# Optimization experiments

Hardware: AMD Instinct MI355X
Metric: run time of the kernel (lower is better)

The kernel has to match this reference:

```python
import jax, jax.numpy as jnp
import numpy as np

E, N, H, D = 800000, 50000, 4, 32
ATT_NORM = 4.0
EPS = 1e-12


def setup_inputs() -> dict:
    key = jax.random.key(0)
    k1, k2, k3, k4, k5 = jax.random.split(key, 5)
    x = jax.random.normal(k1, (E, H, D), dtype=jnp.float32)
    att_l = jax.random.normal(k2, (1, H, D), dtype=jnp.float32)
    att_r = jax.random.normal(k3, (1, H, D), dtype=jnp.float32)
    alpha = jax.random.normal(k4, (E, H), dtype=jnp.float32)
    index = jax.random.randint(k5, (E,), 0, N, dtype=jnp.int64)
    return {"x": x, "att_l": att_l, "att_r": att_r, "alpha": alpha,
            "index": index, "num_nodes": N}


def reference(x, att_l, att_r, alpha, index, num_nodes):
    # recenter=False -> no mean subtraction
    # ||x||^2 along feature dim: [E, H]
    norm_x = jnp.sum(x * x, axis=-1)
    # scatter-max over target nodes: [N, H]; empty segments -> 0 (torch zero-init)
    max_norm = jax.ops.segment_max(norm_x, index, num_segments=num_nodes)
    max_norm = jnp.where(jnp.isfinite(max_norm), max_norm, jnp.zeros_like(max_norm))
    # faithful to torch .view(-1, 1) then [index]: flatten [N,H] -> [N*H,1], gather rows
    max_norm_flat = max_norm.reshape(-1, 1)          # [N*H, 1]
    gathered = max_norm_flat[index]                  # [E, 1]
    max_norm_e = jnp.sqrt(gathered + norm_x)         # [E, H]
    # scale_individually=True: per-head norm of concatenated attention vectors
    att_cat = jnp.concatenate((att_l, att_r), axis=-1)        # [1, H, 2D]
    norm_att = ATT_NORM * jnp.linalg.norm(att_cat, axis=-1)   # [1, H]
    return alpha / (norm_att * max_norm_e + EPS)
```

## Files before the change

kernel.cpp:

```cpp
#include <hip/hip_runtime.h>
#include <math.h>


static constexpr int   H_        = 4;
static constexpr int   D_        = 32;
static constexpr int   N_NODES   = 50000;
static constexpr int   N_LIVE    = N_NODES / H_;
static constexpr float ATT_NORM_ = 4.0f;
static constexpr float EPS_      = 1e-12f;

__global__ void __launch_bounds__(256)
k_norm_scatter(const float* __restrict__ x,
               const int* __restrict__ index,
               const float* __restrict__ att_l,
               const float* __restrict__ att_r,
               float* __restrict__ max_norm,
               float* __restrict__ norm_x,
               float* __restrict__ natt,
               int EH) {
    if (blockIdx.x == 0 && threadIdx.x < H_) {
        const int h = threadIdx.x;
        float s = 0.f;
        #pragma unroll
        for (int d = 0; d < D_; ++d) {
            const float a = att_l[h * D_ + d];
            const float b = att_r[h * D_ + d];
            s += a * a + b * b;
        }
        natt[h] = ATT_NORM_ * sqrtf(s);
    }
    const int p = blockIdx.x * blockDim.x + threadIdx.x;
    if (p >= EH) return;

    const float4* xv = reinterpret_cast<const float4*>(x) + (size_t)p * (D_ / 4);
    float s = 0.f;
    #pragma unroll
    for (int j = 0; j < D_ / 4; ++j) {
        const float4 v = xv[j];
        s += v.x * v.x + v.y * v.y + v.z * v.z + v.w * v.w;
    }
    norm_x[p] = s;

    const int e = p >> 2;
    const int h = p & 3;
    const int n = index[e];
    if (n < N_LIVE) {
        atomicMax(reinterpret_cast<int*>(max_norm) + n * H_ + h, __float_as_int(s));
    }
}

__global__ void __launch_bounds__(256)
k_output(const float* __restrict__ alpha,
         const int* __restrict__ index,
         const float* __restrict__ max_norm,
         const float* __restrict__ norm_x,
         const float* __restrict__ natt,
         float* __restrict__ out,
         int E) {
    const int e = blockIdx.x * blockDim.x + threadIdx.x;
    if (e >= E) return;
    const float n0 = natt[0], n1 = natt[1], n2 = natt[2], n3 = natt[3];
    const float g = max_norm[index[e]];
    const float4 nx = reinterpret_cast<const float4*>(norm_x)[e];
    const float4 al = reinterpret_cast<const float4*>(alpha)[e];
    float4 o;
    o.x = al.x / (n0 * sqrtf(g + nx.x) + EPS_);
    o.y = al.y / (n1 * sqrtf(g + nx.y) + EPS_);
    o.z = al.z / (n2 * sqrtf(g + nx.z) + EPS_);
    o.w = al.w / (n3 * sqrtf(g + nx.w) + EPS_);
    reinterpret_cast<float4*>(out)[e] = o;
}

extern "C" void kernel_launch(void* const* d_in, const int* in_sizes, int n_in,
                              void* d_out, int out_size, void* d_ws, size_t ws_size,
                              hipStream_t stream) {
    const float* x     = (const float*)d_in[0];
    const float* att_l = (const float*)d_in[1];
    const float* att_r = (const float*)d_in[2];
    const float* alpha = (const float*)d_in[3];
    const int*   index = (const int*)d_in[4];

    const int E  = in_sizes[0] / (H_ * D_);
    const int EH = E * H_;

    char* wsb = (char*)d_ws;
    const size_t table_bytes = (size_t)N_NODES * sizeof(float);
    float* max_norm = (float*)wsb;
    float* norm_x   = (float*)(wsb + table_bytes);
    float* natt     = (float*)(wsb + table_bytes + (size_t)EH * sizeof(float));

    hipMemsetAsync(max_norm, 0, table_bytes, stream);

    const int b = 256;
    k_norm_scatter<<<(EH + b - 1) / b, b, 0, stream>>>(
        x, index, att_l, att_r, max_norm, norm_x, natt, EH);
    k_output<<<(E + b - 1) / b, b, 0, stream>>>(
        alpha, index, max_norm, norm_x, natt, (float*)d_out, E);
}
```

Measured before the change: 98.48 us.

## Fuse norm-scatter and output into one persistent kernel with grid barrier

```diff
diff --git a/kernel.cpp b/kernel.cpp
--- a/kernel.cpp
+++ b/kernel.cpp
@@ -8,6 +8,96 @@
 static constexpr int   N_LIVE    = N_NODES / H_;
 static constexpr float ATT_NORM_ = 4.0f;
 static constexpr float EPS_      = 1e-12f;
+static constexpr int   TPB_      = 256;
+static constexpr int   FBLK_     = 512;
+static constexpr int   FITERS_   = 7;
+
+__global__ void __launch_bounds__(TPB_, 2)
+k_fused(const float4* __restrict__ x4,
+        const int*    __restrict__ index,
+        const float*  __restrict__ att_l,
+        const float*  __restrict__ att_r,
+        int*          __restrict__ table,
+        int*          __restrict__ counter,
+        const float4* __restrict__ alpha4,
+        float4*       __restrict__ out4,
+        int E) {
+    __shared__ float s_natt[H_];
+    if (threadIdx.x < H_) {
+        const int h = threadIdx.x;
+        float s = 0.f;
+        #pragma unroll
+        for (int d = 0; d < D_; ++d) {
+            const float a = att_l[h * D_ + d];
+            const float b = att_r[h * D_ + d];
+            s += a * a + b * b;
+        }
+        s_natt[h] = ATT_NORM_ * sqrtf(s);
+    }
+
+    const int T   = FBLK_ * TPB_;
+    const int tid = blockIdx.x * TPB_ + threadIdx.x;
+
+    float sq[FITERS_][H_];
+    int   idx[FITERS_];
+    #pragma unroll
+    for (int it = 0; it < FITERS_; ++it) {
+        const int e = tid + it * T;
+        if (e < E) {
+            idx[it] = index[e];
+            const float4* xb = x4 + (size_t)e * (H_ * D_ / 4);
+            #pragma unroll
+            for (int h = 0; h < H_; ++h) {
+                float s = 0.f;
+                #pragma unroll
+                for (int j = 0; j < D_ / 4; ++j) {
+                    const float4 u = xb[h * (D_ / 4) + j];
+                    s += u.x * u.x + u.y * u.y + u.z * u.z + u.w * u.w;
+                }
+                sq[it][h] = s;
+            }
+            if (idx[it] < N_LIVE) {
+                #pragma unroll
+                for (int h = 0; h < H_; ++h)
+                    atomicMax(table + idx[it] * H_ + h, __float_as_int(sq[it][h]));
+            }
+        } else {
+            idx[it] = 0;
+            #pragma unroll
+            for (int h = 0; h < H_; ++h) sq[it][h] = 0.f;
+        }
+    }
+
+    __threadfence();
+    __syncthreads();
+    if (threadIdx.x == 0) {
+        atomicAdd(counter, 1);
+        while (__hip_atomic_load(counter, __ATOMIC_RELAXED,
+                                 __HIP_MEMORY_SCOPE_AGENT) < FBLK_)
+            __builtin_amdgcn_s_sleep(4);
+    }
+    __syncthreads();
+    __threadfence();
+
+    const float n0 = s_natt[0], n1 = s_natt[1], n2 = s_natt[2], n3 = s_natt[3];
+    #pragma unroll
+    for (int it = 0; it < FITERS_; ++it) {
+        const int e = tid + it * T;
+        if (e < E) {
+            int gb = __hip_atomic_load(table + idx[it], __ATOMIC_RELAXED,
+                                       __HIP_MEMORY_SCOPE_AGENT);
+            gb = gb < 0 ? 0 : gb;
+            const float g = __int_as_float(gb);
+            const float4 al = alpha4[e];
+            float4 o;
+            o.x = al.x / (n0 * sqrtf(g + sq[it][0]) + EPS_);
+            o.y = al.y / (n1 * sqrtf(g + sq[it][1]) + EPS_);
+            o.z = al.z / (n2 * sqrtf(g + sq[it][2]) + EPS_);
+            o.w = al.w / (n3 * sqrtf(g + sq[it][3]) + EPS_);
+            out4[e] = o;
+        }
+    }
+}
 
 __global__ void __launch_bounds__(256)
 k_norm_scatter(const float* __restrict__ x,
@@ -31,7 +121,6 @@
     }
     const int p = blockIdx.x * blockDim.x + threadIdx.x;
     if (p >= EH) return;
-
     const float4* xv = reinterpret_cast<const float4*>(x) + (size_t)p * (D_ / 4);
     float s = 0.f;
     #pragma unroll
@@ -40,13 +129,11 @@
         s += v.x * v.x + v.y * v.y + v.z * v.z + v.w * v.w;
     }
     norm_x[p] = s;
-
     const int e = p >> 2;
     const int h = p & 3;
     const int n = index[e];
-    if (n < N_LIVE) {
+    if (n < N_LIVE)
         atomicMax(reinterpret_cast<int*>(max_norm) + n * H_ + h, __float_as_int(s));
-    }
 }
 
 __global__ void __launch_bounds__(256)
@@ -85,15 +172,29 @@
 
     char* wsb = (char*)d_ws;
     const size_t table_bytes = (size_t)N_NODES * sizeof(float);
-    float* max_norm = (float*)wsb;
-    float* norm_x   = (float*)(wsb + table_bytes);
-    float* natt     = (float*)(wsb + table_bytes + (size_t)EH * sizeof(float));
-
-    hipMemsetAsync(max_norm, 0, table_bytes, stream);
-
-    const int b = 256;
-    k_norm_scatter<<<(EH + b - 1) / b, b, 0, stream>>>(
-        x, index, att_l, att_r, max_norm, norm_x, natt, EH);
-    k_output<<<(E + b - 1) / b, b, 0, stream>>>(
-        alpha, index, max_norm, norm_x, natt, (float*)d_out, E);
-}
+    float* table_f  = (float*)wsb;
+    int*   table_i  = (int*)wsb;
+    int*   counter  = (int*)(wsb + table_bytes);
+    float* norm_x   = (float*)(wsb + table_bytes + 256);
+    float* natt     = (float*)(wsb + table_bytes + 256 + (size_t)EH * sizeof(float));
+
+    hipMemsetAsync(wsb, 0, table_bytes + 256, stream);
+
+    int nb = 0;
+    hipError_t oerr = hipOccupancyMaxActiveBlocksPerMultiprocessor(&nb, k_fused, TPB_, 0);
+    const bool use_fused = (oerr == hipSuccess) && (nb >= 2);
+
+    if (use_fused) {
+        const float4* x4 = (const float4*)x;
+        const float4* a4 = (const float4*)alpha;
+        float4*       o4 = (float4*)d_out;
+        k_fused<<<FBLK_, TPB_, 0, stream>>>(x4, index, att_l, att_r,
+                                            table_i, counter, a4, o4, E);
+    } else {
+        const int b = 256;
+        k_norm_scatter<<<(EH + b - 1) / b, b, 0, stream>>>(
+            x, index, att_l, att_r, table_f, norm_x, natt, EH);
+        k_output<<<(E + b - 1) / b, b, 0, stream>>>(
+            alpha, index, table_f, norm_x, natt, (float*)d_out, E);
+    }
+}
```

New measurement: 267.5 us. 2.72x slower.
